# Kernel tuning notes

Hardware: AMD Instinct MI355X
Metric: run time of the kernel (lower is better)

The kernel has to match this reference:

```python
import jax, jax.numpy as jnp
import numpy as np

D_IN = 512
D_OUT = 512
CONTEXT_LEN = 4096


def setup_inputs() -> dict:
    key = jax.random.key(0)
    kx, kq, kk, kv = jax.random.split(key, 4)
    x = jax.random.normal(kx, (4, 4096, D_IN), dtype=jnp.float32)
    # nn.Linear weights: shape (d_out, d_in), y = x @ W.T (no bias, qkv_bias=False)
    s = 1.0 / np.sqrt(D_IN)
    w_q = jax.random.uniform(kq, (D_OUT, D_IN), dtype=jnp.float32, minval=-s, maxval=s)
    w_k = jax.random.uniform(kk, (D_OUT, D_IN), dtype=jnp.float32, minval=-s, maxval=s)
    w_v = jax.random.uniform(kv, (D_OUT, D_IN), dtype=jnp.float32, minval=-s, maxval=s)
    return {"x": x, "w_q": w_q, "w_k": w_k, "w_v": w_v}


def reference(x, w_q, w_k, w_v):
    b, n, _ = x.shape
    q = jnp.einsum('bnd,od->bno', x, w_q)
    k = jnp.einsum('bnd,od->bno', x, w_k)
    v = jnp.einsum('bnd,od->bno', x, w_v)
    scores = jnp.einsum('bqo,bko->bqk', q, k)  # [b, n, n]
    # Faithful to source: mask buffer is triu(zeros) -> all-False, masked_fill is a no-op.
    mask = jnp.triu(jnp.zeros((CONTEXT_LEN, CONTEXT_LEN), dtype=jnp.float32), k=1).astype(bool)[:n, :n]
    scores = jnp.where(mask, -jnp.inf, scores)
    attn = jax.nn.softmax(scores / np.sqrt(D_OUT).astype(np.float32), axis=-1)
    # dropout rate 0.0 (eval/reference) -> identity
    return jnp.einsum('bqk,bko->bqo', attn, v)
```

## Files before the change

### kernel.cpp

```cpp
#include <hip/hip_runtime.h>
#include <math.h>

typedef __attribute__((ext_vector_type(8))) __bf16 bf16x8;
typedef __attribute__((ext_vector_type(8))) short  short8;
typedef __attribute__((ext_vector_type(4))) unsigned short ushort4v;
typedef __attribute__((ext_vector_type(4))) float  floatx4;
typedef __attribute__((ext_vector_type(16))) float floatx16;

typedef __attribute__((address_space(1))) unsigned int as1_u32;
typedef __attribute__((address_space(3))) unsigned int as3_u32;

__device__ __forceinline__ void async_copy16(const void* g, void* l) {
  __builtin_amdgcn_global_load_lds((const as1_u32*)g, (as3_u32*)l, 16, 0, 0);
}

__device__ __forceinline__ unsigned short f2bf(float f) {
  union { float f; unsigned u; } v; v.f = f;
  unsigned r = v.u + 0x7fffu + ((v.u >> 16) & 1u);
  return (unsigned short)(r >> 16);
}

__device__ __forceinline__ floatx4 mfma_bf16(bf16x8 a, bf16x8 b, floatx4 c) {
  return __builtin_amdgcn_mfma_f32_16x16x32_bf16(a, b, c, 0, 0, 0);
}

__device__ __forceinline__ floatx16 mfma32(bf16x8 a, bf16x8 b, floatx16 c) {
  return __builtin_amdgcn_mfma_f32_32x32x16_bf16(a, b, c, 0, 0, 0);
}

__device__ __forceinline__ bf16x8 lds_frag(const unsigned short* p) {
  return *(const bf16x8*)(const void*)p;
}

__global__ __launch_bounds__(256)
void prep(const float* __restrict__ x,  const float* __restrict__ wq,
          const float* __restrict__ wk, const float* __restrict__ wv,
          unsigned short* __restrict__ Xb, unsigned short* __restrict__ Wqb,
          unsigned short* __restrict__ Wkb, unsigned short* __restrict__ Wvb) {
  const int i = blockIdx.x * 256 + threadIdx.x;
  const float* s; unsigned short* d; int off;
  if (i < 2097152)             { s = x;  d = Xb;  off = i; }
  else if (i < 2097152+65536)  { s = wq; d = Wqb; off = i - 2097152; }
  else if (i < 2097152+131072) { s = wk; d = Wkb; off = i - (2097152+65536); }
  else                         { s = wv; d = Wvb; off = i - (2097152+131072); }
  const float4 v = ((const float4*)s)[off];
  ushort4v o;
  o.x = f2bf(v.x); o.y = f2bf(v.y); o.z = f2bf(v.z); o.w = f2bf(v.w);
  *(ushort4v*)(void*)(d + (size_t)off * 4) = o;
}

__global__ __launch_bounds__(256, 2)
void gemm_qkv(const unsigned short* __restrict__ Xb,
              const unsigned short* __restrict__ Wqb,
              const unsigned short* __restrict__ Wkb,
              const unsigned short* __restrict__ Wvb,
              unsigned short* __restrict__ Q,
              unsigned short* __restrict__ K,
              unsigned short* __restrict__ Vt) {
  const int gid = blockIdx.x;
  const unsigned short *A, *B; unsigned short* C;
  int m0, n0, N;
  if (gid < 512) {
    A = Xb; B = Wqb; C = Q; N = 512;
    m0 = (gid & 127) * 128; n0 = (gid >> 7) * 128;
  } else if (gid < 1024) {
    A = Xb; B = Wkb; C = K; N = 512;
    m0 = ((gid - 512) & 127) * 128; n0 = ((gid - 512) >> 7) * 128;
  } else {
    A = Wvb; B = Xb; C = Vt; N = 16384;
    m0 = ((gid - 1024) & 3) * 128; n0 = ((gid - 1024) >> 2) * 128;
  }

  __shared__ unsigned short As[128 * 64];
  __shared__ unsigned short Bs[128 * 64];
  const int tid = threadIdx.x;
  const int w = tid >> 6, lane = tid & 63;
  const int quad = lane >> 4, l15 = lane & 15;
  const int wm = w >> 1, wn = w & 1;
  const int row_l = lane >> 3;
  const int chk   = lane & 7;
  const int s_chk = chk ^ row_l;

  floatx4 acc[16];
#pragma unroll
  for (int i = 0; i < 16; i++) acc[i] = (floatx4){0.f, 0.f, 0.f, 0.f};

  for (int kt = 0; kt < 8; kt++) {
    __syncthreads();
#pragma unroll
    for (int i = 0; i < 4; i++) {
      const int c = w * 4 + i;
      const int row = c * 8 + row_l;
      async_copy16(A + (size_t)(m0 + row) * 512 + kt * 64 + s_chk * 8, &As[c * 512]);
      async_copy16(B + (size_t)(n0 + row) * 512 + kt * 64 + s_chk * 8, &Bs[c * 512]);
    }
    __syncthreads();
#pragma unroll
    for (int kc = 0; kc < 2; kc++) {
      bf16x8 af[4], bfv[4];
#pragma unroll
      for (int i = 0; i < 4; i++) {
        const int pc = ((kc * 4 + quad) ^ (l15 & 7)) * 8;
        af[i]  = lds_frag(&As[(wm * 64 + i * 16 + l15) * 64 + pc]);
        bfv[i] = lds_frag(&Bs[(wn * 64 + i * 16 + l15) * 64 + pc]);
      }
#pragma unroll
      for (int mi = 0; mi < 4; mi++)
#pragma unroll
        for (int ni = 0; ni < 4; ni++)
          acc[mi * 4 + ni] = mfma_bf16(af[mi], bfv[ni], acc[mi * 4 + ni]);
    }
  }
#pragma unroll
  for (int mi = 0; mi < 4; mi++)
#pragma unroll
    for (int ni = 0; ni < 4; ni++)
#pragma unroll
      for (int r = 0; r < 4; r++) {
        const int row = m0 + wm * 64 + mi * 16 + quad * 4 + r;
        const int col = n0 + wn * 64 + ni * 16 + l15;
        C[(size_t)row * N + col] = f2bf(acc[mi * 4 + ni][r]);
      }
}

#define SCALE 0.044194173824159216f

__global__ __launch_bounds__(512, 1)
void attn_kernel(const unsigned short* __restrict__ Qg,
                 const unsigned short* __restrict__ Kg,
                 const unsigned short* __restrict__ Vt,
                 float* __restrict__ O) {
  __shared__ unsigned short Ks[64 * 512];
  __shared__ unsigned short Vs[512 * 64];
  __shared__ float Sx[64][65];
  __shared__ unsigned short Pb[64 * 64];
  __shared__ float m_row[64], l_row[64], a_row[64];

  const int tid = threadIdx.x;
  const int w = tid >> 6, lane = tid & 63;
  const int l31 = lane & 31, lh = lane >> 5, l7 = lane & 7;

  const int g0 = blockIdx.x;
  const int g  = (g0 & 7) * 32 + (g0 >> 3);
  const int b  = g >> 6;
  const int q0 = (g & 63) * 64;

  if (tid < 64) { m_row[tid] = -3.0e38f; l_row[tid] = 0.f; }

  const int t  = w & 3;
  const int gk = w >> 2;
  const int p2 = w >> 2, dbase = (w & 3) * 128;

  bf16x8 qf[16];
  {
    const unsigned short* qrow =
        Qg + (size_t)(b * 4096 + q0 + (t >> 1) * 32 + l31) * 512;
#pragma unroll
    for (int i = 0; i < 16; i++)
      qf[i] = *(const bf16x8*)(const void*)(qrow + gk * 256 + i * 16 + lh * 8);
  }

  floatx16 oacc[4];
#pragma unroll
  for (int j = 0; j < 4; j++)
#pragma unroll
    for (int r = 0; r < 16; r++) oacc[j][r] = 0.f;

  const unsigned short* kb0 = Kg + (size_t)b * 4096 * 512;
  const unsigned short* vb0 = Vt + (size_t)b * 4096;

  auto issue_K = [&](int kt_) {
#pragma unroll
    for (int u = 0; u < 8; u++) {
      const int row = w * 8 + u;
      async_copy16(kb0 + ((size_t)kt_ * 64 + row) * 512 + (lane ^ u) * 8,
                   &Ks[row * 512]);
    }
  };
  const int v_d = lane >> 3, v_schk = (lane & 7) ^ v_d;
  auto issue_V = [&](int kt_) {
#pragma unroll
    for (int u = 0; u < 8; u++) {
      const int d = w * 64 + u * 8 + v_d;
      async_copy16(vb0 + (size_t)kt_ * 64 + (size_t)d * 16384 + v_schk * 8,
                   &Vs[(w * 64 + u * 8) * 64]);
    }
  };

  const int srow = tid >> 3, sg = tid & 7;
  const int pb_wchunk = sg ^ (srow & 7);

  issue_K(0);

  for (int kt = 0; kt < 64; kt++) {
    asm volatile("s_waitcnt vmcnt(0)" ::: "memory");
    __builtin_amdgcn_sched_barrier(0);
    __syncthreads();
    issue_V(kt);

    {
      floatx16 sa, sb;
#pragma unroll
      for (int r = 0; r < 16; r++) { sa[r] = 0.f; sb[r] = 0.f; }
      const int krow = (t & 1) * 32 + l31;
#pragma unroll
      for (int i = 0; i < 16; i += 2) {
        bf16x8 k0 = lds_frag(&Ks[krow * 512 + (((gk * 32 + i * 2 + lh) ^ l7) * 8)]);
        sa = mfma32(qf[i], k0, sa);
        bf16x8 k1 = lds_frag(&Ks[krow * 512 + (((gk * 32 + i * 2 + 2 + lh) ^ l7) * 8)]);
        sb = mfma32(qf[i + 1], k1, sb);
      }
#pragma unroll
      for (int r = 0; r < 16; r++) sa[r] += sb[r];

      if (w < 4) {
#pragma unroll
        for (int reg = 0; reg < 16; reg++) {
          const int rl = (reg & 3) + 8 * (reg >> 2) + 4 * lh;
          Sx[(t >> 1) * 32 + rl][(t & 1) * 32 + l31] = sa[reg];
        }
      }
      __syncthreads();
      if (w >= 4) {
#pragma unroll
        for (int reg = 0; reg < 16; reg++) {
          const int rl = (reg & 3) + 8 * (reg >> 2) + 4 * lh;
          float* p = &Sx[(t >> 1) * 32 + rl][(t & 1) * 32 + l31];
          *p = (*p + sa[reg]) * SCALE;
        }
      }
    }
    __syncthreads();

    {
      float vals[8];
      float tmax = -3.0e38f;
#pragma unroll
      for (int j = 0; j < 8; j++) {
        float xv = Sx[srow][sg * 8 + j];
        xv = fminf(fmaxf(xv, -1.0e4f), 1.0e4f);
        vals[j] = xv;
        tmax = fmaxf(tmax, xv);
      }
      tmax = fmaxf(tmax, __shfl_xor(tmax, 1));
      tmax = fmaxf(tmax, __shfl_xor(tmax, 2));
      tmax = fmaxf(tmax, __shfl_xor(tmax, 4));
      const float m_old = m_row[srow];
      const float m_new = fmaxf(m_old, tmax);
      const float alpha = __expf(m_old - m_new);
      float lsum = 0.f;
      short8 pvec;
#pragma unroll
      for (int j = 0; j < 8; j++) {
        const float p = __expf(vals[j] - m_new);
        lsum += p;
        pvec[j] = (short)f2bf(p);
      }
      lsum += __shfl_xor(lsum, 1);
      lsum += __shfl_xor(lsum, 2);
      lsum += __shfl_xor(lsum, 4);
      *(short8*)(void*)&Pb[srow * 64 + pb_wchunk * 8] = pvec;
      if (sg == 0) {
        m_row[srow] = m_new;
        l_row[srow] = l_row[srow] * alpha + lsum;
        a_row[srow] = alpha;
      }
    }
    __syncthreads();

#pragma unroll
    for (int reg = 0; reg < 16; reg++) {
      const float a = a_row[p2 * 32 + (reg & 3) + 8 * (reg >> 2) + 4 * lh];
#pragma unroll
      for (int j = 0; j < 4; j++) oacc[j][reg] *= a;
    }
    bf16x8 pfr[4];
    {
      const int q = p2 * 32 + l31;
#pragma unroll
      for (int kk = 0; kk < 4; kk++)
        pfr[kk] = lds_frag(&Pb[q * 64 + (((kk * 2 + lh) ^ l7) * 8)]);
    }

    asm volatile("s_waitcnt vmcnt(0)" ::: "memory");
    __builtin_amdgcn_sched_barrier(0);
    __syncthreads();
    if (kt < 63) issue_K(kt + 1);

#pragma unroll
    for (int j = 0; j < 4; j++) {
      const int d = dbase + j * 32 + l31;
#pragma unroll
      for (int kk = 0; kk < 4; kk++) {
        bf16x8 vfr = lds_frag(&Vs[d * 64 + (((kk * 2 + lh) ^ l7) * 8)]);
        oacc[j] = mfma32(pfr[kk], vfr, oacc[j]);
      }
    }
  }

  __syncthreads();
#pragma unroll
  for (int reg = 0; reg < 16; reg++) {
    const int rl = (reg & 3) + 8 * (reg >> 2) + 4 * lh;
    const float inv = 1.0f / l_row[p2 * 32 + rl];
    const int row = b * 4096 + q0 + p2 * 32 + rl;
#pragma unroll
    for (int j = 0; j < 4; j++)
      O[(size_t)row * 512 + dbase + j * 32 + l31] = oacc[j][reg] * inv;
  }
}

extern "C" void kernel_launch(void* const* d_in, const int* in_sizes, int n_in,
                              void* d_out, int out_size, void* d_ws, size_t ws_size,
                              hipStream_t stream) {
  const float* x   = (const float*)d_in[0];
  const float* wqf = (const float*)d_in[1];
  const float* wkf = (const float*)d_in[2];
  const float* wvf = (const float*)d_in[3];

  unsigned short* Xb  = (unsigned short*)d_out;
  unsigned short* Wqb = (unsigned short*)d_ws;
  unsigned short* Wkb = Wqb + (size_t)512 * 512;
  unsigned short* Wvb = Wkb + (size_t)512 * 512;
  unsigned short* Q   = Wvb + (size_t)512 * 512;
  unsigned short* K   = Q + (size_t)16384 * 512;
  unsigned short* Vt  = K + (size_t)16384 * 512;

  prep<<<dim3(8960), 256, 0, stream>>>(x, wqf, wkf, wvf, Xb, Wqb, Wkb, Wvb);
  gemm_qkv<<<dim3(1536), 256, 0, stream>>>(Xb, Wqb, Wkb, Wvb, Q, K, Vt);
  attn_kernel<<<dim3(256), 512, 0, stream>>>(Q, K, Vt, (float*)d_out);
}
```

Measured before the change: 336.5 us.

## Load K and V MFMA fragments directly from global memory instead of LDS staging

Removes the LDS buffers for K and V and the async global-to-LDS copies with their waits and barriers. Each wave now reads its own K and V fragments straight from global memory into registers, using a small rotating prefetch of four fragments. This cuts LDS traffic and block-wide syncs, but each K/V tile is now fetched separately by several waves, so global and L2 traffic rises and load latency is exposed to the MFMA chain.

```diff
diff --git a/kernel.cpp b/kernel.cpp
--- a/kernel.cpp
+++ b/kernel.cpp
@@ -29,6 +29,10 @@
 }
 
 __device__ __forceinline__ bf16x8 lds_frag(const unsigned short* p) {
+  return *(const bf16x8*)(const void*)p;
+}
+
+__device__ __forceinline__ bf16x8 g_frag(const unsigned short* p) {
   return *(const bf16x8*)(const void*)p;
 }
 
@@ -130,8 +134,6 @@
                  const unsigned short* __restrict__ Kg,
                  const unsigned short* __restrict__ Vt,
                  float* __restrict__ O) {
-  __shared__ unsigned short Ks[64 * 512];
-  __shared__ unsigned short Vs[512 * 64];
   __shared__ float Sx[64][65];
   __shared__ unsigned short Pb[64 * 64];
   __shared__ float m_row[64], l_row[64], a_row[64];
@@ -157,7 +159,7 @@
         Qg + (size_t)(b * 4096 + q0 + (t >> 1) * 32 + l31) * 512;
 #pragma unroll
     for (int i = 0; i < 16; i++)
-      qf[i] = *(const bf16x8*)(const void*)(qrow + gk * 256 + i * 16 + lh * 8);
+      qf[i] = g_frag(qrow + gk * 256 + i * 16 + lh * 8);
   }
 
   floatx16 oacc[4];
@@ -166,49 +168,31 @@
 #pragma unroll
     for (int r = 0; r < 16; r++) oacc[j][r] = 0.f;
 
-  const unsigned short* kb0 = Kg + (size_t)b * 4096 * 512;
-  const unsigned short* vb0 = Vt + (size_t)b * 4096;
-
-  auto issue_K = [&](int kt_) {
-#pragma unroll
-    for (int u = 0; u < 8; u++) {
-      const int row = w * 8 + u;
-      async_copy16(kb0 + ((size_t)kt_ * 64 + row) * 512 + (lane ^ u) * 8,
-                   &Ks[row * 512]);
-    }
-  };
-  const int v_d = lane >> 3, v_schk = (lane & 7) ^ v_d;
-  auto issue_V = [&](int kt_) {
-#pragma unroll
-    for (int u = 0; u < 8; u++) {
-      const int d = w * 64 + u * 8 + v_d;
-      async_copy16(vb0 + (size_t)kt_ * 64 + (size_t)d * 16384 + v_schk * 8,
-                   &Vs[(w * 64 + u * 8) * 64]);
-    }
-  };
+  const unsigned short* kfb = Kg + (size_t)b * 4096 * 512
+      + (size_t)((t & 1) * 32 + l31) * 512 + gk * 256 + lh * 8;
+  const unsigned short* vfb = Vt + (size_t)b * 4096
+      + (size_t)(dbase + l31) * 16384 + lh * 8;
 
   const int srow = tid >> 3, sg = tid & 7;
   const int pb_wchunk = sg ^ (srow & 7);
 
-  issue_K(0);
-
   for (int kt = 0; kt < 64; kt++) {
-    asm volatile("s_waitcnt vmcnt(0)" ::: "memory");
-    __builtin_amdgcn_sched_barrier(0);
-    __syncthreads();
-    issue_V(kt);
-
     {
       floatx16 sa, sb;
 #pragma unroll
       for (int r = 0; r < 16; r++) { sa[r] = 0.f; sb[r] = 0.f; }
-      const int krow = (t & 1) * 32 + l31;
+      const unsigned short* kp = kfb + (size_t)kt * (64 * 512);
+      bf16x8 kf[4];
+#pragma unroll
+      for (int i = 0; i < 4; i++) kf[i] = g_frag(kp + i * 16);
 #pragma unroll
       for (int i = 0; i < 16; i += 2) {
-        bf16x8 k0 = lds_frag(&Ks[krow * 512 + (((gk * 32 + i * 2 + lh) ^ l7) * 8)]);
-        sa = mfma32(qf[i], k0, sa);
-        bf16x8 k1 = lds_frag(&Ks[krow * 512 + (((gk * 32 + i * 2 + 2 + lh) ^ l7) * 8)]);
-        sb = mfma32(qf[i + 1], k1, sb);
+        bf16x8 c0 = kf[i & 3];
+        bf16x8 c1 = kf[(i + 1) & 3];
+        if (i + 4 < 16) kf[i & 3]       = g_frag(kp + (i + 4) * 16);
+        if (i + 5 < 16) kf[(i + 1) & 3] = g_frag(kp + (i + 5) * 16);
+        sa = mfma32(qf[i], c0, sa);
+        sb = mfma32(qf[i + 1], c1, sb);
       }
 #pragma unroll
       for (int r = 0; r < 16; r++) sa[r] += sb[r];
@@ -282,18 +266,19 @@
         pfr[kk] = lds_frag(&Pb[q * 64 + (((kk * 2 + lh) ^ l7) * 8)]);
     }
 
-    asm volatile("s_waitcnt vmcnt(0)" ::: "memory");
-    __builtin_amdgcn_sched_barrier(0);
-    __syncthreads();
-    if (kt < 63) issue_K(kt + 1);
-
-#pragma unroll
-    for (int j = 0; j < 4; j++) {
-      const int d = dbase + j * 32 + l31;
-#pragma unroll
-      for (int kk = 0; kk < 4; kk++) {
-        bf16x8 vfr = lds_frag(&Vs[d * 64 + (((kk * 2 + lh) ^ l7) * 8)]);
-        oacc[j] = mfma32(pfr[kk], vfr, oacc[j]);
+    {
+      const unsigned short* vp = vfb + kt * 64;
+      bf16x8 vf[4];
+#pragma unroll
+      for (int u = 0; u < 4; u++) vf[u] = g_frag(vp + u * 16);
+#pragma unroll
+      for (int u = 0; u < 16; u++) {
+        bf16x8 cur = vf[u & 3];
+        if (u + 4 < 16) {
+          const int un = u + 4;
+          vf[u & 3] = g_frag(vp + (size_t)(un >> 2) * (32 * 16384) + (un & 3) * 16);
+        }
+        oacc[u >> 2] = mfma32(pfr[u & 3], cur, oacc[u >> 2]);
       }
     }
   }
```

Result: slower. 704.1 us (+109.2%).

## Software-pipeline QK and PV MFMAs across tiles and change LDS swizzle

Applied to the files above, without the earlier changes.

Restructures the attention main loop so the QK^T MFMAs for tile kt+1 are interleaved with the PV MFMAs for tile kt, with a peeled prologue and epilogue. K and V async loads are issued one stage earlier, reducing the number of vmcnt waits and barriers per iteration. It also changes the LDS XOR swizzle to a row-plus-row/8 hash, aiming to cut bank conflicts. Register pressure goes up, since pfr and both accumulator sets are live together, and K/V buffer reuse now relies on the new barrier placement.

```diff
diff --git a/kernel.cpp b/kernel.cpp
--- a/kernel.cpp
+++ b/kernel.cpp
@@ -138,18 +138,43 @@
 
   const int tid = threadIdx.x;
   const int w = tid >> 6, lane = tid & 63;
-  const int l31 = lane & 31, lh = lane >> 5, l7 = lane & 7;
+  const int l31 = lane & 31, lh = lane >> 5;
 
   const int g0 = blockIdx.x;
   const int g  = (g0 & 7) * 32 + (g0 >> 3);
   const int b  = g >> 6;
   const int q0 = (g & 63) * 64;
 
-  if (tid < 64) { m_row[tid] = -3.0e38f; l_row[tid] = 0.f; }
-
   const int t  = w & 3;
   const int gk = w >> 2;
   const int p2 = w >> 2, dbase = (w & 3) * 128;
+
+  const unsigned short* kb0 = Kg + (size_t)b * 4096 * 512;
+  const unsigned short* vb0 = Vt + (size_t)b * 4096;
+  const int v_d = lane >> 3;
+
+  auto issue_K = [&](int kt_) {
+#pragma unroll
+    for (int u = 0; u < 8; u++) {
+      const int row = w * 8 + u;
+      const int hk = (u + w) & 7;
+      async_copy16(kb0 + ((size_t)kt_ * 64 + row) * 512 + (lane ^ hk) * 8,
+                   &Ks[row * 512]);
+    }
+  };
+  auto issue_V = [&](int kt_) {
+#pragma unroll
+    for (int u = 0; u < 8; u++) {
+      const int d = w * 64 + u * 8 + v_d;
+      const int hv = (v_d + u) & 7;
+      async_copy16(vb0 + (size_t)kt_ * 64 + (size_t)d * 16384 + ((lane & 7) ^ hv) * 8,
+                   &Vs[(w * 64 + u * 8) * 64]);
+    }
+  };
+
+  issue_K(0);
+
+  if (tid < 64) { m_row[tid] = -3.0e38f; l_row[tid] = 0.f; }
 
   bf16x8 qf[16];
   {
@@ -166,136 +191,171 @@
 #pragma unroll
     for (int r = 0; r < 16; r++) oacc[j][r] = 0.f;
 
-  const unsigned short* kb0 = Kg + (size_t)b * 4096 * 512;
-  const unsigned short* vb0 = Vt + (size_t)b * 4096;
-
-  auto issue_K = [&](int kt_) {
-#pragma unroll
-    for (int u = 0; u < 8; u++) {
-      const int row = w * 8 + u;
-      async_copy16(kb0 + ((size_t)kt_ * 64 + row) * 512 + (lane ^ u) * 8,
-                   &Ks[row * 512]);
+  const int krow = (t & 1) * 32 + l31;
+  const int hKr  = ((krow & 7) + (krow >> 3)) & 7;
+  const int srow = tid >> 3, sg = tid & 7;
+  const int pb_wc = sg ^ (((srow & 7) + (srow >> 3)) & 7);
+  const int pq   = p2 * 32 + l31;
+  const int hPq  = ((pq & 7) + (pq >> 3)) & 7;
+
+  bf16x8 pfr[4];
+
+  asm volatile("s_waitcnt vmcnt(0)" ::: "memory");
+  __builtin_amdgcn_sched_barrier(0);
+  __syncthreads();
+  issue_V(0);
+
+  {
+    floatx16 sa, sb;
+#pragma unroll
+    for (int r = 0; r < 16; r++) { sa[r] = 0.f; sb[r] = 0.f; }
+#pragma unroll
+    for (int i = 0; i < 16; i += 2) {
+      bf16x8 k0 = lds_frag(&Ks[krow * 512 + (((gk * 32 + i * 2 + lh) ^ hKr) * 8)]);
+      sa = mfma32(qf[i], k0, sa);
+      bf16x8 k1 = lds_frag(&Ks[krow * 512 + (((gk * 32 + i * 2 + 2 + lh) ^ hKr) * 8)]);
+      sb = mfma32(qf[i + 1], k1, sb);
+    }
+#pragma unroll
+    for (int r = 0; r < 16; r++) sa[r] += sb[r];
+    if (w < 4) {
+#pragma unroll
+      for (int reg = 0; reg < 16; reg++) {
+        const int rl = (reg & 3) + 8 * (reg >> 2) + 4 * lh;
+        Sx[(t >> 1) * 32 + rl][(t & 1) * 32 + l31] = sa[reg];
+      }
+    }
+    __syncthreads();
+    if (w >= 4) {
+#pragma unroll
+      for (int reg = 0; reg < 16; reg++) {
+        const int rl = (reg & 3) + 8 * (reg >> 2) + 4 * lh;
+        float* p = &Sx[(t >> 1) * 32 + rl][(t & 1) * 32 + l31];
+        *p = (*p + sa[reg]) * SCALE;
+      }
+    }
+    issue_K(1);
+  }
+  __syncthreads();
+
+  auto softmax_step = [&]() {
+    float vals[8];
+    float tmax = -3.0e38f;
+#pragma unroll
+    for (int j = 0; j < 8; j++) {
+      float xv = Sx[srow][sg * 8 + j];
+      xv = fminf(fmaxf(xv, -1.0e4f), 1.0e4f);
+      vals[j] = xv;
+      tmax = fmaxf(tmax, xv);
+    }
+    tmax = fmaxf(tmax, __shfl_xor(tmax, 1));
+    tmax = fmaxf(tmax, __shfl_xor(tmax, 2));
+    tmax = fmaxf(tmax, __shfl_xor(tmax, 4));
+    const float m_old = m_row[srow];
+    const float m_new = fmaxf(m_old, tmax);
+    const float alpha = __expf(m_old - m_new);
+    float lsum = 0.f;
+    short8 pvec;
+#pragma unroll
+    for (int j = 0; j < 8; j++) {
+      const float p = __expf(vals[j] - m_new);
+      lsum += p;
+      pvec[j] = (short)f2bf(p);
+    }
+    lsum += __shfl_xor(lsum, 1);
+    lsum += __shfl_xor(lsum, 2);
+    lsum += __shfl_xor(lsum, 4);
+    *(short8*)(void*)&Pb[srow * 64 + pb_wc * 8] = pvec;
+    if (sg == 0) {
+      m_row[srow] = m_new;
+      l_row[srow] = l_row[srow] * alpha + lsum;
+      a_row[srow] = alpha;
     }
   };
-  const int v_d = lane >> 3, v_schk = (lane & 7) ^ v_d;
-  auto issue_V = [&](int kt_) {
-#pragma unroll
-    for (int u = 0; u < 8; u++) {
-      const int d = w * 64 + u * 8 + v_d;
-      async_copy16(vb0 + (size_t)kt_ * 64 + (size_t)d * 16384 + v_schk * 8,
-                   &Vs[(w * 64 + u * 8) * 64]);
-    }
+  auto prep_pv = [&]() {
+#pragma unroll
+    for (int reg = 0; reg < 16; reg++) {
+      const float a = a_row[p2 * 32 + (reg & 3) + 8 * (reg >> 2) + 4 * lh];
+#pragma unroll
+      for (int j = 0; j < 4; j++) oacc[j][reg] *= a;
+    }
+#pragma unroll
+    for (int kk = 0; kk < 4; kk++)
+      pfr[kk] = lds_frag(&Pb[pq * 64 + (((kk * 2 + lh) ^ hPq) * 8)]);
   };
 
-  const int srow = tid >> 3, sg = tid & 7;
-  const int pb_wchunk = sg ^ (srow & 7);
-
-  issue_K(0);
-
-  for (int kt = 0; kt < 64; kt++) {
+  softmax_step();
+  __syncthreads();
+  prep_pv();
+
+  for (int kt = 0; kt < 63; kt++) {
     asm volatile("s_waitcnt vmcnt(0)" ::: "memory");
     __builtin_amdgcn_sched_barrier(0);
     __syncthreads();
-    issue_V(kt);
-
-    {
-      floatx16 sa, sb;
-#pragma unroll
-      for (int r = 0; r < 16; r++) { sa[r] = 0.f; sb[r] = 0.f; }
-      const int krow = (t & 1) * 32 + l31;
-#pragma unroll
-      for (int i = 0; i < 16; i += 2) {
-        bf16x8 k0 = lds_frag(&Ks[krow * 512 + (((gk * 32 + i * 2 + lh) ^ l7) * 8)]);
-        sa = mfma32(qf[i], k0, sa);
-        bf16x8 k1 = lds_frag(&Ks[krow * 512 + (((gk * 32 + i * 2 + 2 + lh) ^ l7) * 8)]);
-        sb = mfma32(qf[i + 1], k1, sb);
-      }
-#pragma unroll
-      for (int r = 0; r < 16; r++) sa[r] += sb[r];
-
-      if (w < 4) {
-#pragma unroll
-        for (int reg = 0; reg < 16; reg++) {
-          const int rl = (reg & 3) + 8 * (reg >> 2) + 4 * lh;
-          Sx[(t >> 1) * 32 + rl][(t & 1) * 32 + l31] = sa[reg];
-        }
-      }
-      __syncthreads();
-      if (w >= 4) {
-#pragma unroll
-        for (int reg = 0; reg < 16; reg++) {
-          const int rl = (reg & 3) + 8 * (reg >> 2) + 4 * lh;
-          float* p = &Sx[(t >> 1) * 32 + rl][(t & 1) * 32 + l31];
-          *p = (*p + sa[reg]) * SCALE;
-        }
-      }
-    }
-    __syncthreads();
-
-    {
-      float vals[8];
-      float tmax = -3.0e38f;
-#pragma unroll
-      for (int j = 0; j < 8; j++) {
-        float xv = Sx[srow][sg * 8 + j];
-        xv = fminf(fmaxf(xv, -1.0e4f), 1.0e4f);
-        vals[j] = xv;
-        tmax = fmaxf(tmax, xv);
-      }
-      tmax = fmaxf(tmax, __shfl_xor(tmax, 1));
-      tmax = fmaxf(tmax, __shfl_xor(tmax, 2));
-      tmax = fmaxf(tmax, __shfl_xor(tmax, 4));
-      const float m_old = m_row[srow];
-      const float m_new = fmaxf(m_old, tmax);
-      const float alpha = __expf(m_old - m_new);
-      float lsum = 0.f;
-      short8 pvec;
-#pragma unroll
-      for (int j = 0; j < 8; j++) {
-        const float p = __expf(vals[j] - m_new);
-        lsum += p;
-        pvec[j] = (short)f2bf(p);
-      }
-      lsum += __shfl_xor(lsum, 1);
-      lsum += __shfl_xor(lsum, 2);
-      lsum += __shfl_xor(lsum, 4);
-      *(short8*)(void*)&Pb[srow * 64 + pb_wchunk * 8] = pvec;
-      if (sg == 0) {
-        m_row[srow] = m_new;
-        l_row[srow] = l_row[srow] * alpha + lsum;
-        a_row[srow] = alpha;
-      }
-    }
-    __syncthreads();
-
-#pragma unroll
-    for (int reg = 0; reg < 16; reg++) {
-      const float a = a_row[p2 * 32 + (reg & 3) + 8 * (reg >> 2) + 4 * lh];
-#pragma unroll
-      for (int j = 0; j < 4; j++) oacc[j][reg] *= a;
-    }
-    bf16x8 pfr[4];
-    {
-      const int q = p2 * 32 + l31;
-#pragma unroll
-      for (int kk = 0; kk < 4; kk++)
-        pfr[kk] = lds_frag(&Pb[q * 64 + (((kk * 2 + lh) ^ l7) * 8)]);
-    }
-
-    asm volatile("s_waitcnt vmcnt(0)" ::: "memory");
-    __builtin_amdgcn_sched_barrier(0);
-    __syncthreads();
-    if (kt < 63) issue_K(kt + 1);
-
-#pragma unroll
-    for (int j = 0; j < 4; j++) {
-      const int d = dbase + j * 32 + l31;
-#pragma unroll
-      for (int kk = 0; kk < 4; kk++) {
-        bf16x8 vfr = lds_frag(&Vs[d * 64 + (((kk * 2 + lh) ^ l7) * 8)]);
+
+    floatx16 sa, sb;
+#pragma unroll
+    for (int r = 0; r < 16; r++) { sa[r] = 0.f; sb[r] = 0.f; }
+#pragma unroll
+    for (int i = 0; i < 16; i += 2) {
+      bf16x8 k0 = lds_frag(&Ks[krow * 512 + (((gk * 32 + i * 2 + lh) ^ hKr) * 8)]);
+      sa = mfma32(qf[i], k0, sa);
+      {
+        const int j = i >> 2, kk = i & 3;
+        const int d = dbase + j * 32 + l31;
+        const int hV = ((d & 7) + (d >> 3)) & 7;
+        bf16x8 vfr = lds_frag(&Vs[d * 64 + (((kk * 2 + lh) ^ hV) * 8)]);
         oacc[j] = mfma32(pfr[kk], vfr, oacc[j]);
       }
-    }
+      bf16x8 k1 = lds_frag(&Ks[krow * 512 + (((gk * 32 + i * 2 + 2 + lh) ^ hKr) * 8)]);
+      sb = mfma32(qf[i + 1], k1, sb);
+      {
+        const int u = i + 1;
+        const int j = u >> 2, kk = u & 3;
+        const int d = dbase + j * 32 + l31;
+        const int hV = ((d & 7) + (d >> 3)) & 7;
+        bf16x8 vfr = lds_frag(&Vs[d * 64 + (((kk * 2 + lh) ^ hV) * 8)]);
+        oacc[j] = mfma32(pfr[kk], vfr, oacc[j]);
+      }
+    }
+#pragma unroll
+    for (int r = 0; r < 16; r++) sa[r] += sb[r];
+
+    if (w < 4) {
+#pragma unroll
+      for (int reg = 0; reg < 16; reg++) {
+        const int rl = (reg & 3) + 8 * (reg >> 2) + 4 * lh;
+        Sx[(t >> 1) * 32 + rl][(t & 1) * 32 + l31] = sa[reg];
+      }
+    }
+    __syncthreads();
+    if (w >= 4) {
+#pragma unroll
+      for (int reg = 0; reg < 16; reg++) {
+        const int rl = (reg & 3) + 8 * (reg >> 2) + 4 * lh;
+        float* p = &Sx[(t >> 1) * 32 + rl][(t & 1) * 32 + l31];
+        *p = (*p + sa[reg]) * SCALE;
+      }
+    }
+    issue_V(kt + 1);
+    if (kt + 2 <= 63) issue_K(kt + 2);
+    __syncthreads();
+
+    softmax_step();
+    __syncthreads();
+    prep_pv();
+  }
+
+  asm volatile("s_waitcnt vmcnt(0)" ::: "memory");
+  __builtin_amdgcn_sched_barrier(0);
+  __syncthreads();
+#pragma unroll
+  for (int u = 0; u < 16; u++) {
+    const int j = u >> 2, kk = u & 3;
+    const int d = dbase + j * 32 + l31;
+    const int hV = ((d & 7) + (d >> 3)) & 7;
+    bf16x8 vfr = lds_frag(&Vs[d * 64 + (((kk * 2 + lh) ^ hV) * 8)]);
+    oacc[j] = mfma32(pfr[kk], vfr, oacc[j]);
   }
 
   __syncthreads();
```

Result: slower. 474.1 us (+40.9%).
